# Optimization experiments

Hardware: AMD Instinct MI355X
Metric: run time of the kernel (lower is better)

## Reference

```python
import jax, jax.numpy as jnp
import numpy as np

B, T, E, U, V = 64, 100, 512, 512, 32000


def gru_layer(xs_tm, Wg, bg, Wc, bc):
    """TF GRUCell math. xs_tm: [T, B, D]. Returns (ys [T,B,U], h_final [B,U])."""
    u_dim = Wc.shape[1]
    h0 = jnp.zeros((xs_tm.shape[1], u_dim), xs_tm.dtype)

    def step(h, x):
        ru = jax.nn.sigmoid(jnp.concatenate([x, h], -1) @ Wg + bg)
        r, u = jnp.split(ru, 2, axis=-1)
        c = jnp.tanh(jnp.concatenate([x, r * h], -1) @ Wc + bc)
        h_new = u * h + (1.0 - u) * c
        return h_new, h_new

    h_final, ys = jax.lax.scan(step, h0, xs_tm)
    return ys, h_final


def setup_inputs() -> dict:
    key = jax.random.key(0)
    ks = jax.random.split(key, 16)

    def w(k, shape):
        fan_in = shape[0]
        return jax.random.normal(k, shape, jnp.float32) * (1.0 / np.sqrt(fan_in))

    inp = {
        "x": jax.random.randint(ks[0], (B, T), 0, V, jnp.int32),
        "embedding": jax.random.normal(ks[1], (V, E), jnp.float32) * 0.02,
        # bi-directional layer, input dim E
        "Wg_fw": w(ks[2], (E + U, 2 * U)), "bg_fw": jnp.ones((2 * U,), jnp.float32),
        "Wc_fw": w(ks[3], (E + U, U)),     "bc_fw": jnp.zeros((U,), jnp.float32),
        "Wg_bw": w(ks[4], (E + U, 2 * U)), "bg_bw": jnp.ones((2 * U,), jnp.float32),
        "Wc_bw": w(ks[5], (E + U, U)),     "bc_bw": jnp.zeros((U,), jnp.float32),
        # uni layer 1, input dim 2U (concat fw/bw)
        "Wg_u1": w(ks[6], (2 * U + U, 2 * U)), "bg_u1": jnp.ones((2 * U,), jnp.float32),
        "Wc_u1": w(ks[7], (2 * U + U, U)),     "bc_u1": jnp.zeros((U,), jnp.float32),
        # uni layer 2, input dim U
        "Wg_u2": w(ks[8], (U + U, 2 * U)), "bg_u2": jnp.ones((2 * U,), jnp.float32),
        "Wc_u2": w(ks[9], (U + U, U)),     "bc_u2": jnp.zeros((U,), jnp.float32),
    }
    return inp


def reference(x, embedding, Wg_fw, bg_fw, Wc_fw, bc_fw, Wg_bw, bg_bw, Wc_bw, bc_bw,
              Wg_u1, bg_u1, Wc_u1, bc_u1, Wg_u2, bg_u2, Wc_u2, bc_u2):
    emb = embedding[x]                      # [B, T, E] embedding lookup
    xs = jnp.swapaxes(emb, 0, 1)            # [T, B, E] time-major for scan
    # bidirectional GRU layer
    yf, _ = gru_layer(xs, Wg_fw, bg_fw, Wc_fw, bc_fw)
    yb, _ = gru_layer(xs[::-1], Wg_bw, bg_bw, Wc_bw, bc_bw)
    a = jnp.concatenate([yf, yb[::-1]], -1)  # [T, B, 2U]
    # 2-layer unidirectional GRU stack (MultiRNNCell)
    a, s1 = gru_layer(a, Wg_u1, bg_u1, Wc_u1, bc_u1)
    a, s2 = gru_layer(a, Wg_u2, bg_u2, Wc_u2, bc_u2)
    output = jnp.swapaxes(a, 0, 1)          # [B, T, U]
    state = jnp.stack([s1, s2])             # [2, B, U] per-layer final states
    return output, state
```

## Files before the change

### kernel.cpp

```cpp
#include <hip/hip_runtime.h>
#include <hip/hip_bf16.h>


#define TT 100

using f32x4 = __attribute__((ext_vector_type(4))) float;
using s16x8 = __attribute__((ext_vector_type(8))) short;
using u32x4 = __attribute__((ext_vector_type(4))) unsigned;

__device__ __forceinline__ unsigned short f2bfu(float x) {
  __hip_bfloat16 b = __float2bfloat16(x);
  unsigned short u;
  __builtin_memcpy(&u, &b, sizeof(u));
  return u;
}
__device__ __forceinline__ float bfu2f(unsigned short u) {
  __hip_bfloat16 b;
  __builtin_memcpy(&b, &u, sizeof(b));
  return __bfloat162float(b);
}
__device__ __forceinline__ float sigm(float x) {
  x = fminf(fmaxf(x, -30.f), 30.f);
  return 1.f / (1.f + __expf(-x));
}
__device__ __forceinline__ float tanh_fast(float x) {
  x = fminf(fmaxf(x, -15.f), 15.f);
  float e = __expf(-2.f * x);
  return (1.f - e) / (1.f + e);
}
__device__ __forceinline__ void vm_drain() {
  asm volatile("s_waitcnt vmcnt(0)" ::: "memory");
}

__global__ __launch_bounds__(256) void pack_w_kernel(const float* __restrict__ Wg,
                                                     const float* __restrict__ Wc,
                                                     int ldg, int ldc, int ktTot,
                                                     unsigned short* __restrict__ hi,
                                                     unsigned short* __restrict__ lo) {
  const int gg = blockIdx.x * 256 + threadIdx.x;
  if (gg >= 96 * ktTot * 64) return;
  const int lane = gg & 63;
  const int pair = gg >> 6;
  const int kt = pair % ktTot;
  const int nt = pair / ktTot;
  const int kg = lane >> 4;
  const int nl = lane & 15;
  const size_t off = (size_t)gg * 8;
  for (int i = 0; i < 8; ++i) {
    const int k = kt * 32 + kg * 8 + i;
    float v = (nt < 64) ? Wg[(size_t)k * ldg + nt * 16 + nl]
                        : Wc[(size_t)k * ldc + (nt - 64) * 16 + nl];
    unsigned short h = f2bfu(v);
    hi[off + i] = h;
    lo[off + i] = f2bfu(v - bfu2f(h));
  }
}

template <int ASRC>
__global__ __launch_bounds__(256) void gemm_mfma(
    const int* __restrict__ xtok, const float* __restrict__ emb,
    const unsigned short* __restrict__ aHi, const unsigned short* __restrict__ aLo, int lda,
    const unsigned short* __restrict__ bHi, const unsigned short* __restrict__ bLo,
    int ktTot, int ktX,
    const float* __restrict__ bg, const float* __restrict__ bc,
    float* __restrict__ C) {
  __shared__ unsigned short Ah[128 * 40];
  __shared__ unsigned short Al[128 * 40];

  const int tid = threadIdx.x;
  const int lane = tid & 63;
  const int w = tid >> 6;
  const int bm = blockIdx.x, bn = blockIdx.y;
  const int fm = lane & 15, fkg = lane >> 4;

  const int arow = tid >> 1;
  const int koff = (tid & 1) * 16;
  const int rowg = bm * 128 + arow;
  int embIdx = 0;
  if (ASRC == 0) {
    const int t_ = rowg >> 6, b_ = rowg & 63;
    embIdx = xtok[b_ * TT + t_];
  }

  f32x4 acc[2][8];
#pragma unroll
  for (int rt = 0; rt < 2; ++rt)
#pragma unroll
    for (int ni = 0; ni < 8; ++ni) acc[rt][ni] = (f32x4){0.f, 0.f, 0.f, 0.f};

  for (int kt = 0; kt < ktX; ++kt) {
    __syncthreads();
    if (ASRC == 0) {
      const float* src = emb + (size_t)embIdx * 512 + kt * 32 + koff;
      s16x8 h0, h1, l0, l1;
#pragma unroll
      for (int c = 0; c < 2; ++c) {
        f32x4 va = *(const f32x4*)(src + c * 8);
        f32x4 vb = *(const f32x4*)(src + c * 8 + 4);
        s16x8 hh, ll;
#pragma unroll
        for (int j = 0; j < 4; ++j) {
          unsigned short h = f2bfu(va[j]);
          hh[j] = (short)h; ll[j] = (short)f2bfu(va[j] - bfu2f(h));
          unsigned short h2 = f2bfu(vb[j]);
          hh[j + 4] = (short)h2; ll[j + 4] = (short)f2bfu(vb[j] - bfu2f(h2));
        }
        if (c == 0) { h0 = hh; l0 = ll; } else { h1 = hh; l1 = ll; }
      }
      *(s16x8*)(Ah + arow * 40 + koff) = h0;
      *(s16x8*)(Ah + arow * 40 + koff + 8) = h1;
      *(s16x8*)(Al + arow * 40 + koff) = l0;
      *(s16x8*)(Al + arow * 40 + koff + 8) = l1;
    } else {
      const size_t so = (size_t)rowg * lda + kt * 32 + koff;
      s16x8 h0 = *(const s16x8*)(aHi + so);
      s16x8 h1 = *(const s16x8*)(aHi + so + 8);
      s16x8 l0 = *(const s16x8*)(aLo + so);
      s16x8 l1 = *(const s16x8*)(aLo + so + 8);
      *(s16x8*)(Ah + arow * 40 + koff) = h0;
      *(s16x8*)(Ah + arow * 40 + koff + 8) = h1;
      *(s16x8*)(Al + arow * 40 + koff) = l0;
      *(s16x8*)(Al + arow * 40 + koff + 8) = l1;
    }
    __syncthreads();

    s16x8 ah[2], al[2];
#pragma unroll
    for (int rt = 0; rt < 2; ++rt) {
      const int m = w * 32 + rt * 16 + fm;
      ah[rt] = *(const s16x8*)(Ah + m * 40 + fkg * 8);
      al[rt] = *(const s16x8*)(Al + m * 40 + fkg * 8);
    }
#pragma unroll
    for (int ni = 0; ni < 8; ++ni) {
      const int nt = bn * 8 + ni;
      const size_t bo = ((size_t)nt * ktTot + kt) * 512 + lane * 8;
      s16x8 bh = *(const s16x8*)(bHi + bo);
      s16x8 bl = *(const s16x8*)(bLo + bo);
#pragma unroll
      for (int rt = 0; rt < 2; ++rt) {
        acc[rt][ni] = __builtin_amdgcn_mfma_f32_16x16x32_bf16(ah[rt], bh, acc[rt][ni], 0, 0, 0);
        acc[rt][ni] = __builtin_amdgcn_mfma_f32_16x16x32_bf16(ah[rt], bl, acc[rt][ni], 0, 0, 0);
        acc[rt][ni] = __builtin_amdgcn_mfma_f32_16x16x32_bf16(al[rt], bh, acc[rt][ni], 0, 0, 0);
      }
    }
  }

#pragma unroll
  for (int ni = 0; ni < 8; ++ni) {
    const int nt = bn * 8 + ni;
    int dcol; float bias;
    if (nt < 64) { dcol = nt * 16 + fm; bias = bg[dcol]; }
    else { dcol = 1024 + (nt - 64) * 16 + fm; bias = bc[(nt - 64) * 16 + fm]; }
#pragma unroll
    for (int rt = 0; rt < 2; ++rt)
#pragma unroll
      for (int j = 0; j < 4; ++j) {
        const int row = bm * 128 + w * 32 + rt * 16 + fkg * 4 + j;
        C[(size_t)row * 1536 + dcol] = acc[rt][ni][j] + bias;
      }
  }
}

template <int NB>
__global__ __launch_bounds__(256, 1) void gru_scan_kernel(
    const float* __restrict__ gxF, const float* __restrict__ gxB,
    const unsigned short* __restrict__ wHiF, const unsigned short* __restrict__ wLoF,
    const unsigned short* __restrict__ wHiB, const unsigned short* __restrict__ wLoB,
    int ktTot, int ktH0,
    unsigned* __restrict__ hPkG, unsigned* __restrict__ rPkG,
    unsigned* __restrict__ slots,
    unsigned short* __restrict__ yHi, unsigned short* __restrict__ yLo, int yld,
    float* __restrict__ outb,
    float* __restrict__ stout) {
  __shared__ unsigned short wHi_s[3 * 8192];
  __shared__ unsigned short wLo_s[3 * 8192];
  __shared__ float scr[4][16][17];
  __shared__ float scr2[4][16][17];

  const int tid = threadIdx.x;
  const int lane = tid & 63;
  const int wv = tid >> 6;
  const int bid = blockIdx.x;
  const int g = bid & 7;
  const int wg = bid >> 3;
  const int hs = wg << 4;

  int dir = 0, b0;
  const float* gx;
  const unsigned short *wph, *wpl;
  if (NB == 16) {
    dir = g & 1;
    b0 = (g >> 1) << 4;
    gx = dir ? gxB : gxF;
    wph = dir ? wHiB : wHiF;
    wpl = dir ? wLoB : wLoF;
  } else {
    b0 = g * NB;
    gx = gxF;
    wph = wHiF;
    wpl = wLoF;
  }

  {
    const int nt0[3] = {wg, 32 + wg, 64 + wg};
    for (int c = 0; c < 3; ++c) {
      const unsigned short* sH = wph + ((size_t)nt0[c] * ktTot + ktH0) * 512;
      const unsigned short* sL = wpl + ((size_t)nt0[c] * ktTot + ktH0) * 512;
      unsigned short* dH = wHi_s + c * 8192;
      unsigned short* dL = wLo_s + c * 8192;
#pragma unroll
      for (int it = 0; it < 4; ++it) {
        const int o = (it * 256 + tid) * 8;
        *(s16x8*)(dH + o) = *(const s16x8*)(sH + o);
        *(s16x8*)(dL + o) = *(const s16x8*)(sL + o);
      }
    }
  }
  __syncthreads();

  unsigned* gslots = slots + g * 32;

  const int fm = lane & 15;
  const int fkg = lane >> 4;
  const int afe = fm * 512;
  const int asw = (fm & 7) << 3;

  const int ob = tid >> 4, oj = tid & 15;
  const bool own = (ob < NB);
  const int ui = ob * 512 + ((hs + oj) ^ ((ob & 7) << 3));

  const size_t tileo = (size_t)g * 8192;

  auto mfma_regs = [&](int cidx, const s16x8* ah, const s16x8* al,
                       float (*dst)[16][17]) {
    f32x4 acc0 = {0.f, 0.f, 0.f, 0.f}, acc1 = {0.f, 0.f, 0.f, 0.f};
#pragma unroll
    for (int q = 0; q < 4; ++q) {
      const int kt = wv * 4 + q;
      const int wo = ((cidx * 16 + kt) * 64 + lane) * 8;
      s16x8 bh = *(const s16x8*)(wHi_s + wo);
      s16x8 bl = *(const s16x8*)(wLo_s + wo);
      if (q & 1) {
        acc1 = __builtin_amdgcn_mfma_f32_16x16x32_bf16(ah[q], bh, acc1, 0, 0, 0);
        acc1 = __builtin_amdgcn_mfma_f32_16x16x32_bf16(ah[q], bl, acc1, 0, 0, 0);
        acc1 = __builtin_amdgcn_mfma_f32_16x16x32_bf16(al[q], bh, acc1, 0, 0, 0);
      } else {
        acc0 = __builtin_amdgcn_mfma_f32_16x16x32_bf16(ah[q], bh, acc0, 0, 0, 0);
        acc0 = __builtin_amdgcn_mfma_f32_16x16x32_bf16(ah[q], bl, acc0, 0, 0, 0);
        acc0 = __builtin_amdgcn_mfma_f32_16x16x32_bf16(al[q], bh, acc0, 0, 0, 0);
      }
    }
#pragma unroll
    for (int j = 0; j < 4; ++j) dst[wv][fkg * 4 + j][fm] = acc0[j] + acc1[j];
  };

  auto load_frags = [&](const unsigned* pk, s16x8* ah, s16x8* al,
                        bool withHv, unsigned* hvOut) {
    u32x4 d[4][2];
#pragma unroll
    for (int q = 0; q < 4; ++q) {
      const int kt = wv * 4 + q;
      const unsigned* p = pk + tileo + afe + ((kt * 32 + fkg * 8) ^ asw);
      asm volatile("global_load_dwordx4 %0, %1, off sc0 sc1"
                   : "=v"(d[q][0]) : "v"(p) : "memory");
      asm volatile("global_load_dwordx4 %0, %1, off sc0 sc1"
                   : "=v"(d[q][1]) : "v"(p + 4) : "memory");
    }
    if (withHv && own)
      asm volatile("global_load_dword %0, %1, off sc0 sc1"
                   : "=v"(*hvOut) : "v"(pk + tileo + ui) : "memory");
    vm_drain();
    __builtin_amdgcn_sched_barrier(0);
#pragma unroll
    for (int q = 0; q < 4; ++q) {
      u32x4 hh, ll;
#pragma unroll
      for (int i = 0; i < 2; ++i) {
        const u32x4 dd = d[q][i];
        hh[2 * i] = (dd[0] & 0xffffu) | (dd[1] << 16);
        hh[2 * i + 1] = (dd[2] & 0xffffu) | (dd[3] << 16);
        ll[2 * i] = (dd[0] >> 16) | (dd[1] & 0xffff0000u);
        ll[2 * i + 1] = (dd[2] >> 16) | (dd[3] & 0xffff0000u);
      }
      __builtin_memcpy(&ah[q], &hh, 16);
      __builtin_memcpy(&al[q], &ll, 16);
    }
  };

  auto poll = [&](unsigned target) {
    if (tid < 32) {
      const unsigned* p = gslots + tid;
      unsigned v;
      do {
        asm volatile("global_load_dword %0, %1, off sc0 sc1\n\ts_waitcnt vmcnt(0)"
                     : "=v"(v) : "v"(p) : "memory");
      } while (!__all(v >= target));
    }
    __syncthreads();
  };

  float gxr = 0.f, gxu = 0.f, gxc = 0.f;
  if (own) {
    const float* row = gx + ((size_t)(dir ? TT - 1 : 0) * 64 + b0 + ob) * 1536 + hs + oj;
    gxr = row[0]; gxu = row[512]; gxc = row[1024];
  }

  for (int t = 0; t < TT; ++t) {
    const int tg = dir ? (TT - 1 - t) : t;

    s16x8 ah[4], al[4];
    unsigned hvu = 0;
    load_frags(hPkG, ah, al, true, &hvu);
    mfma_regs(0, ah, al, scr);
    __syncthreads();

    float hv = 0.f;
    if (own) {
      float rpre = scr[0][ob][oj] + scr[1][ob][oj] + scr[2][ob][oj] + scr[3][ob][oj] + gxr;
      float sg = sigm(rpre);
      hv = bfu2f((unsigned short)(hvu & 0xffffu)) + bfu2f((unsigned short)(hvu >> 16));
      float rh = sg * hv;
      unsigned short hh_ = f2bfu(rh);
      unsigned short ll_ = f2bfu(rh - bfu2f(hh_));
      unsigned e = (unsigned)hh_ | ((unsigned)ll_ << 16);
      asm volatile("global_store_dword %0, %1, off sc0 sc1"
                   :: "v"(rPkG + tileo + ui), "v"(e) : "memory");
    }
    vm_drain();
    __syncthreads();
    if (tid == 0) {
      unsigned tv = 2 * t + 1;
      asm volatile("global_store_dword %0, %1, off sc0 sc1"
                   :: "v"(gslots + wg), "v"(tv) : "memory");
    }

    mfma_regs(1, ah, al, scr2);

    float ngxr = 0.f, ngxu = 0.f, ngxc = 0.f;
    if (own && t + 1 < TT) {
      const int tgn = dir ? (TT - 2 - t) : (t + 1);
      const float* row = gx + ((size_t)tgn * 64 + b0 + ob) * 1536 + hs + oj;
      ngxr = row[0]; ngxu = row[512]; ngxc = row[1024];
    }

    poll(2 * t + 1);

    load_frags(rPkG, ah, al, false, nullptr);
    mfma_regs(2, ah, al, scr);
    __syncthreads();

    float hn = 0.f;
    unsigned short hh_ = 0, ll_ = 0;
    if (own) {
      float upre = scr2[0][ob][oj] + scr2[1][ob][oj] + scr2[2][ob][oj] + scr2[3][ob][oj] + gxu;
      float uv = sigm(upre);
      float cpre = scr[0][ob][oj] + scr[1][ob][oj] + scr[2][ob][oj] + scr[3][ob][oj] + gxc;
      float cv = tanh_fast(cpre);
      hn = uv * hv + (1.f - uv) * cv;
      hh_ = f2bfu(hn);
      ll_ = f2bfu(hn - bfu2f(hh_));
    }

    if (t == TT - 1) {
      if (own) {
        if (yHi) {
          const int ycol = (NB == 16) ? (dir * 512 + hs + oj) : (hs + oj);
          const size_t yi = ((size_t)tg * 64 + (b0 + ob)) * yld + ycol;
          yHi[yi] = hh_; yLo[yi] = ll_;
        }
        if (outb) outb[((size_t)(b0 + ob) * TT + t) * 512 + hs + oj] = hn;
        if (stout) stout[(size_t)(b0 + ob) * 512 + hs + oj] = hn;
      }
      break;
    }

    if (own) {
      unsigned e = (unsigned)hh_ | ((unsigned)ll_ << 16);
      asm volatile("global_store_dword %0, %1, off sc0 sc1"
                   :: "v"(hPkG + tileo + ui), "v"(e) : "memory");
    }
    vm_drain();
    __syncthreads();
    if (tid == 0) {
      unsigned tv = 2 * t + 2;
      asm volatile("global_store_dword %0, %1, off sc0 sc1"
                   :: "v"(gslots + wg), "v"(tv) : "memory");
    }

    if (own) {
      if (yHi) {
        const int ycol = (NB == 16) ? (dir * 512 + hs + oj) : (hs + oj);
        const size_t yi = ((size_t)tg * 64 + (b0 + ob)) * yld + ycol;
        yHi[yi] = hh_; yLo[yi] = ll_;
      }
      if (outb) outb[((size_t)(b0 + ob) * TT + t) * 512 + hs + oj] = hn;
    }
    gxr = ngxr; gxu = ngxu; gxc = ngxc;

    poll(2 * t + 2);
  }
}

extern "C" void kernel_launch(void* const* d_in, const int* in_sizes, int n_in,
                              void* d_out, int out_size, void* d_ws, size_t ws_size,
                              hipStream_t stream) {
  (void)in_sizes; (void)n_in; (void)out_size; (void)ws_size;
  const int* x = (const int*)d_in[0];
  const float* emb = (const float*)d_in[1];
  const float* WgFw = (const float*)d_in[2];
  const float* bgFw = (const float*)d_in[3];
  const float* WcFw = (const float*)d_in[4];
  const float* bcFw = (const float*)d_in[5];
  const float* WgBw = (const float*)d_in[6];
  const float* bgBw = (const float*)d_in[7];
  const float* WcBw = (const float*)d_in[8];
  const float* bcBw = (const float*)d_in[9];
  const float* WgU1 = (const float*)d_in[10];
  const float* bgU1 = (const float*)d_in[11];
  const float* WcU1 = (const float*)d_in[12];
  const float* bcU1 = (const float*)d_in[13];
  const float* WgU2 = (const float*)d_in[14];
  const float* bgU2 = (const float*)d_in[15];
  const float* WcU2 = (const float*)d_in[16];
  const float* bcU2 = (const float*)d_in[17];

  char* ws = (char*)d_ws;
  float* bufA = (float*)(ws + 0);
  float* bufB = (float*)(ws + 39321600);
  unsigned short* ycatHi = (unsigned short*)(ws + 78643200);
  unsigned short* ycatLo = (unsigned short*)(ws + 91750400);
  unsigned short* y1Hi = (unsigned short*)(ws + 78643200);
  unsigned short* y1Lo = (unsigned short*)(ws + 85196800);
  unsigned short* wpFwHi = (unsigned short*)(ws + 104857600);
  unsigned short* wpFwLo = (unsigned short*)(ws + 108003328);
  unsigned short* wpBwHi = (unsigned short*)(ws + 111149056);
  unsigned short* wpBwLo = (unsigned short*)(ws + 114294784);
  unsigned short* wpU1Hi = (unsigned short*)(ws + 117440512);
  unsigned short* wpU1Lo = (unsigned short*)(ws + 122159104);
  unsigned short* wpU2Hi = (unsigned short*)(ws + 117440512);
  unsigned short* wpU2Lo = (unsigned short*)(ws + 120586240);
  unsigned* hPkG = (unsigned*)(ws + 126877696);
  unsigned* rPkG = (unsigned*)(ws + 127139840);
  unsigned* bars = (unsigned*)(ws + 127401984);

  float* out = (float*)d_out;
  float* st1 = out + (size_t)64 * TT * 512;
  float* st2 = st1 + 64 * 512;

  hipMemsetAsync(bars, 0, 4096, stream);

  pack_w_kernel<<<768, 256, 0, stream>>>(WgFw, WcFw, 1024, 512, 32, wpFwHi, wpFwLo);
  pack_w_kernel<<<768, 256, 0, stream>>>(WgBw, WcBw, 1024, 512, 32, wpBwHi, wpBwLo);
  pack_w_kernel<<<1152, 256, 0, stream>>>(WgU1, WcU1, 1024, 512, 48, wpU1Hi, wpU1Lo);

  gemm_mfma<0><<<dim3(50, 12), 256, 0, stream>>>(
      x, emb, nullptr, nullptr, 0, wpFwHi, wpFwLo, 32, 16, bgFw, bcFw, bufA);
  gemm_mfma<0><<<dim3(50, 12), 256, 0, stream>>>(
      x, emb, nullptr, nullptr, 0, wpBwHi, wpBwLo, 32, 16, bgBw, bcBw, bufB);

  hipMemsetAsync(hPkG, 0, 524288, stream);
  {
    const float *a0 = bufA, *a1 = bufB;
    const unsigned short *w0 = wpFwHi, *w1 = wpFwLo, *w2 = wpBwHi, *w3 = wpBwLo;
    int ktT = 32, ktH = 16;
    unsigned *h0 = hPkG, *r0 = rPkG;
    unsigned* bp = bars;
    unsigned short *yh = ycatHi, *yl = ycatLo; int yld = 1024;
    float *on = nullptr, *sn = nullptr;
    void* args[] = {&a0, &a1, &w0, &w1, &w2, &w3, &ktT, &ktH, &h0, &r0,
                    &bp, &yh, &yl, &yld, &on, &sn};
    hipLaunchCooperativeKernel((const void*)gru_scan_kernel<16>, dim3(256), dim3(256),
                               args, 0, stream);
  }

  gemm_mfma<1><<<dim3(50, 12), 256, 0, stream>>>(
      nullptr, nullptr, ycatHi, ycatLo, 1024, wpU1Hi, wpU1Lo, 48, 32, bgU1, bcU1, bufA);

  hipMemsetAsync(hPkG, 0, 524288, stream);
  {
    const float *a0 = bufA, *a1 = nullptr;
    const unsigned short *w0 = wpU1Hi, *w1 = wpU1Lo, *w2 = nullptr, *w3 = nullptr;
    int ktT = 48, ktH = 32;
    unsigned *h0 = hPkG, *r0 = rPkG;
    unsigned* bp = bars + 256;
    unsigned short *yh = y1Hi, *yl = y1Lo; int yld = 512;
    float *on = nullptr, *sn = st1;
    void* args[] = {&a0, &a1, &w0, &w1, &w2, &w3, &ktT, &ktH, &h0, &r0,
                    &bp, &yh, &yl, &yld, &on, &sn};
    hipLaunchCooperativeKernel((const void*)gru_scan_kernel<8>, dim3(256), dim3(256),
                               args, 0, stream);
  }

  pack_w_kernel<<<768, 256, 0, stream>>>(WgU2, WcU2, 1024, 512, 32, wpU2Hi, wpU2Lo);

  gemm_mfma<1><<<dim3(50, 12), 256, 0, stream>>>(
      nullptr, nullptr, y1Hi, y1Lo, 512, wpU2Hi, wpU2Lo, 32, 16, bgU2, bcU2, bufB);

  hipMemsetAsync(hPkG, 0, 524288, stream);
  {
    const float *a0 = bufB, *a1 = nullptr;
    const unsigned short *w0 = wpU2Hi, *w1 = wpU2Lo, *w2 = nullptr, *w3 = nullptr;
    int ktT = 32, ktH = 16;
    unsigned *h0 = hPkG, *r0 = rPkG;
    unsigned* bp = bars + 512;
    unsigned short *yh = nullptr, *yl = nullptr; int yld = 0;
    float *on = out, *sn = st2;
    void* args[] = {&a0, &a1, &w0, &w1, &w2, &w3, &ktT, &ktH, &h0, &r0,
                    &bp, &yh, &yl, &yld, &on, &sn};
    hipLaunchCooperativeKernel((const void*)gru_scan_kernel<8>, dim3(256), dim3(256),
                               args, 0, stream);
  }
}
```

Before: 1.810 ms.

## Fuse the two unidirectional GRU layers into one wavefront-pipelined cooperative kernel

Replaces the separate layer-1 scan, layer-2 input GEMM and layer-2 scan with a single cooperative kernel. Half the blocks run layer 1 and the other half run layer 2, which polls layer-1 step flags and computes its input projection per timestep with global-memory weights. The layers thus overlap in a time-skewed pipeline, removing a full serial scan plus a GEMM launch. The cost is 128 blocks per layer instead of 256, extra per-step work for the fused input projection, and cross-layer flag polling latency.

```diff
diff --git a/kernel.cpp b/kernel.cpp
--- a/kernel.cpp
+++ b/kernel.cpp
@@ -30,6 +30,9 @@
 }
 __device__ __forceinline__ void vm_drain() {
   asm volatile("s_waitcnt vmcnt(0)" ::: "memory");
+}
+__device__ __forceinline__ void sc1_store_b16(void* p, unsigned v) {
+  asm volatile("global_store_short %0, %1, off sc0 sc1" :: "v"(p), "v"(v) : "memory");
 }
 
 __global__ __launch_bounds__(256) void pack_w_kernel(const float* __restrict__ Wg,
@@ -399,6 +402,324 @@
     gxr = ngxr; gxu = ngxu; gxc = ngxc;
 
     poll(2 * t + 2);
+  }
+}
+
+__global__ __launch_bounds__(256, 1) void uni_fused_kernel(
+    const float* __restrict__ gx1,
+    const unsigned short* __restrict__ w1Hi, const unsigned short* __restrict__ w1Lo,
+    const unsigned short* __restrict__ w2Hi, const unsigned short* __restrict__ w2Lo,
+    const float* __restrict__ bg2, const float* __restrict__ bc2,
+    unsigned* __restrict__ hPk1, unsigned* __restrict__ rPk1,
+    unsigned* __restrict__ hPk2, unsigned* __restrict__ rPk2,
+    unsigned* __restrict__ slots1, unsigned* __restrict__ slots2,
+    unsigned short* __restrict__ y1Hi, unsigned short* __restrict__ y1Lo,
+    float* __restrict__ out, float* __restrict__ st1, float* __restrict__ st2) {
+  __shared__ unsigned short wHi_s[3 * 8192];
+  __shared__ unsigned short wLo_s[3 * 8192];
+  __shared__ float scr[4][16][17];
+  __shared__ float scr2[4][16][17];
+  __shared__ float scr3[4][16][17];
+
+  const int tid = threadIdx.x;
+  const int lane = tid & 63;
+  const int wv = tid >> 6;
+  const int bid = blockIdx.x;
+  const int role = (bid >= 128);
+  const int g = (bid & 127) >> 5;
+  const int wg = bid & 31;
+  const int hs = wg << 4;
+  const int b0 = g * 16;
+
+  const unsigned short* wph = role ? w2Hi : w1Hi;
+  const unsigned short* wpl = role ? w2Lo : w1Lo;
+  const int ktTot = role ? 32 : 48;
+  const int ktH0 = role ? 16 : 32;
+  unsigned* hPk = role ? hPk2 : hPk1;
+  unsigned* rPk = role ? rPk2 : rPk1;
+  unsigned* myslots = (role ? slots2 : slots1) + g * 32;
+  unsigned* u1gs = slots1 + g * 32;
+
+  {
+    const int nt0[3] = {wg, 32 + wg, 64 + wg};
+    for (int c = 0; c < 3; ++c) {
+      const unsigned short* sH = wph + ((size_t)nt0[c] * ktTot + ktH0) * 512;
+      const unsigned short* sL = wpl + ((size_t)nt0[c] * ktTot + ktH0) * 512;
+      unsigned short* dH = wHi_s + c * 8192;
+      unsigned short* dL = wLo_s + c * 8192;
+#pragma unroll
+      for (int it = 0; it < 4; ++it) {
+        const int o = (it * 256 + tid) * 8;
+        *(s16x8*)(dH + o) = *(const s16x8*)(sH + o);
+        *(s16x8*)(dL + o) = *(const s16x8*)(sL + o);
+      }
+    }
+  }
+  __syncthreads();
+
+  const int fm = lane & 15;
+  const int fkg = lane >> 4;
+  const int afe = fm * 512;
+  const int asw = (fm & 7) << 3;
+  const int ob = tid >> 4, oj = tid & 15;
+  const int ui = ob * 512 + ((hs + oj) ^ ((ob & 7) << 3));
+  const size_t tileo = (size_t)g * 8192;
+
+  auto mfma_regs = [&](int cidx, const s16x8* ah, const s16x8* al,
+                       float (*dst)[16][17]) {
+    f32x4 acc0 = {0.f, 0.f, 0.f, 0.f}, acc1 = {0.f, 0.f, 0.f, 0.f};
+#pragma unroll
+    for (int q = 0; q < 4; ++q) {
+      const int kt = wv * 4 + q;
+      const int wo = ((cidx * 16 + kt) * 64 + lane) * 8;
+      s16x8 bh = *(const s16x8*)(wHi_s + wo);
+      s16x8 bl = *(const s16x8*)(wLo_s + wo);
+      if (q & 1) {
+        acc1 = __builtin_amdgcn_mfma_f32_16x16x32_bf16(ah[q], bh, acc1, 0, 0, 0);
+        acc1 = __builtin_amdgcn_mfma_f32_16x16x32_bf16(ah[q], bl, acc1, 0, 0, 0);
+        acc1 = __builtin_amdgcn_mfma_f32_16x16x32_bf16(al[q], bh, acc1, 0, 0, 0);
+      } else {
+        acc0 = __builtin_amdgcn_mfma_f32_16x16x32_bf16(ah[q], bh, acc0, 0, 0, 0);
+        acc0 = __builtin_amdgcn_mfma_f32_16x16x32_bf16(ah[q], bl, acc0, 0, 0, 0);
+        acc0 = __builtin_amdgcn_mfma_f32_16x16x32_bf16(al[q], bh, acc0, 0, 0, 0);
+      }
+    }
+#pragma unroll
+    for (int j = 0; j < 4; ++j) dst[wv][fkg * 4 + j][fm] = acc0[j] + acc1[j];
+  };
+
+  auto mfma_xp = [&](int cidx, const s16x8* ah, const s16x8* al,
+                     float (*dst)[16][17]) {
+    const int nt0[3] = {wg, 32 + wg, 64 + wg};
+    f32x4 acc0 = {0.f, 0.f, 0.f, 0.f}, acc1 = {0.f, 0.f, 0.f, 0.f};
+#pragma unroll
+    for (int q = 0; q < 4; ++q) {
+      const int kt = wv * 4 + q;
+      const size_t bo = ((size_t)nt0[cidx] * 32 + kt) * 512 + lane * 8;
+      s16x8 bh = *(const s16x8*)(w2Hi + bo);
+      s16x8 bl = *(const s16x8*)(w2Lo + bo);
+      if (q & 1) {
+        acc1 = __builtin_amdgcn_mfma_f32_16x16x32_bf16(ah[q], bh, acc1, 0, 0, 0);
+        acc1 = __builtin_amdgcn_mfma_f32_16x16x32_bf16(ah[q], bl, acc1, 0, 0, 0);
+        acc1 = __builtin_amdgcn_mfma_f32_16x16x32_bf16(al[q], bh, acc1, 0, 0, 0);
+      } else {
+        acc0 = __builtin_amdgcn_mfma_f32_16x16x32_bf16(ah[q], bh, acc0, 0, 0, 0);
+        acc0 = __builtin_amdgcn_mfma_f32_16x16x32_bf16(ah[q], bl, acc0, 0, 0, 0);
+        acc0 = __builtin_amdgcn_mfma_f32_16x16x32_bf16(al[q], bh, acc0, 0, 0, 0);
+      }
+    }
+#pragma unroll
+    for (int j = 0; j < 4; ++j) dst[wv][fkg * 4 + j][fm] = acc0[j] + acc1[j];
+  };
+
+  auto load_frags = [&](const unsigned* pk, s16x8* ah, s16x8* al,
+                        bool withHv, unsigned* hvOut) {
+    u32x4 d[4][2];
+#pragma unroll
+    for (int q = 0; q < 4; ++q) {
+      const int kt = wv * 4 + q;
+      const unsigned* p = pk + tileo + afe + ((kt * 32 + fkg * 8) ^ asw);
+      asm volatile("global_load_dwordx4 %0, %1, off sc0 sc1"
+                   : "=v"(d[q][0]) : "v"(p) : "memory");
+      asm volatile("global_load_dwordx4 %0, %1, off sc0 sc1"
+                   : "=v"(d[q][1]) : "v"(p + 4) : "memory");
+    }
+    if (withHv)
+      asm volatile("global_load_dword %0, %1, off sc0 sc1"
+                   : "=v"(*hvOut) : "v"(pk + tileo + ui) : "memory");
+    vm_drain();
+    __builtin_amdgcn_sched_barrier(0);
+#pragma unroll
+    for (int q = 0; q < 4; ++q) {
+      u32x4 hh, ll;
+#pragma unroll
+      for (int i = 0; i < 2; ++i) {
+        const u32x4 dd = d[q][i];
+        hh[2 * i] = (dd[0] & 0xffffu) | (dd[1] << 16);
+        hh[2 * i + 1] = (dd[2] & 0xffffu) | (dd[3] << 16);
+        ll[2 * i] = (dd[0] >> 16) | (dd[1] & 0xffff0000u);
+        ll[2 * i + 1] = (dd[2] >> 16) | (dd[3] & 0xffff0000u);
+      }
+      __builtin_memcpy(&ah[q], &hh, 16);
+      __builtin_memcpy(&al[q], &ll, 16);
+    }
+  };
+
+  auto poll_arr = [&](const unsigned* arr, unsigned target) {
+    if (tid < 32) {
+      const unsigned* p = arr + tid;
+      unsigned v;
+      do {
+        asm volatile("global_load_dword %0, %1, off sc0 sc1\n\ts_waitcnt vmcnt(0)"
+                     : "=v"(v) : "v"(p) : "memory");
+      } while (!__all(v >= target));
+    }
+    __syncthreads();
+  };
+
+  if (role == 0) {
+    float gxr, gxu, gxc;
+    {
+      const float* row = gx1 + ((size_t)0 * 64 + b0 + ob) * 1536 + hs + oj;
+      gxr = row[0]; gxu = row[512]; gxc = row[1024];
+    }
+    for (int t = 0; t < TT; ++t) {
+      s16x8 ah[4], al[4];
+      unsigned hvu = 0;
+      load_frags(hPk, ah, al, true, &hvu);
+      mfma_regs(0, ah, al, scr);
+      __syncthreads();
+
+      float rpre = scr[0][ob][oj] + scr[1][ob][oj] + scr[2][ob][oj] + scr[3][ob][oj] + gxr;
+      float sg = sigm(rpre);
+      float hv = bfu2f((unsigned short)(hvu & 0xffffu)) + bfu2f((unsigned short)(hvu >> 16));
+      float rh = sg * hv;
+      {
+        unsigned short hh_ = f2bfu(rh);
+        unsigned short ll_ = f2bfu(rh - bfu2f(hh_));
+        unsigned e = (unsigned)hh_ | ((unsigned)ll_ << 16);
+        asm volatile("global_store_dword %0, %1, off sc0 sc1"
+                     :: "v"(rPk + tileo + ui), "v"(e) : "memory");
+      }
+      vm_drain();
+      __syncthreads();
+      if (tid == 0) {
+        unsigned tv = 2 * t + 1;
+        asm volatile("global_store_dword %0, %1, off sc0 sc1"
+                     :: "v"(myslots + wg), "v"(tv) : "memory");
+      }
+
+      mfma_regs(1, ah, al, scr2);
+
+      float ngxr = 0.f, ngxu = 0.f, ngxc = 0.f;
+      if (t + 1 < TT) {
+        const float* row = gx1 + ((size_t)(t + 1) * 64 + b0 + ob) * 1536 + hs + oj;
+        ngxr = row[0]; ngxu = row[512]; ngxc = row[1024];
+      }
+
+      poll_arr(myslots, 2 * t + 1);
+
+      load_frags(rPk, ah, al, false, nullptr);
+      mfma_regs(2, ah, al, scr);
+      __syncthreads();
+
+      float upre = scr2[0][ob][oj] + scr2[1][ob][oj] + scr2[2][ob][oj] + scr2[3][ob][oj] + gxu;
+      float uv = sigm(upre);
+      float cpre = scr[0][ob][oj] + scr[1][ob][oj] + scr[2][ob][oj] + scr[3][ob][oj] + gxc;
+      float hn = uv * hv + (1.f - uv) * tanh_fast(cpre);
+      unsigned short hh_ = f2bfu(hn);
+      unsigned short ll_ = f2bfu(hn - bfu2f(hh_));
+
+      {
+        const size_t yi = ((size_t)t * 64 + (b0 + ob)) * 512 + hs + oj;
+        sc1_store_b16(y1Hi + yi, hh_);
+        sc1_store_b16(y1Lo + yi, ll_);
+      }
+      if (t < TT - 1) {
+        unsigned e = (unsigned)hh_ | ((unsigned)ll_ << 16);
+        asm volatile("global_store_dword %0, %1, off sc0 sc1"
+                     :: "v"(hPk + tileo + ui), "v"(e) : "memory");
+      } else {
+        st1[(size_t)(b0 + ob) * 512 + hs + oj] = hn;
+      }
+      vm_drain();
+      __syncthreads();
+      if (tid == 0) {
+        unsigned tv = 2 * t + 2;
+        asm volatile("global_store_dword %0, %1, off sc0 sc1"
+                     :: "v"(myslots + wg), "v"(tv) : "memory");
+      }
+      if (t == TT - 1) break;
+      gxr = ngxr; gxu = ngxu; gxc = ngxc;
+      poll_arr(myslots, 2 * t + 2);
+    }
+  } else {
+    const float br = bg2[hs + oj], bu = bg2[512 + hs + oj], bc_ = bc2[hs + oj];
+    for (int t = 0; t < TT; ++t) {
+      poll_arr(u1gs, 2 * t + 2);
+
+      s16x8 xh[4], xl[4];
+      {
+#pragma unroll
+        for (int q = 0; q < 4; ++q) {
+          const int kt = wv * 4 + q;
+          const size_t yo = ((size_t)t * 64 + b0 + fm) * 512 + kt * 32 + fkg * 8;
+          asm volatile("global_load_dwordx4 %0, %1, off sc0 sc1"
+                       : "=v"(xh[q]) : "v"(y1Hi + yo) : "memory");
+          asm volatile("global_load_dwordx4 %0, %1, off sc0 sc1"
+                       : "=v"(xl[q]) : "v"(y1Lo + yo) : "memory");
+        }
+        vm_drain();
+        __builtin_amdgcn_sched_barrier(0);
+      }
+      mfma_xp(0, xh, xl, scr);
+      mfma_xp(1, xh, xl, scr2);
+      mfma_xp(2, xh, xl, scr3);
+      __syncthreads();
+      float gxr = scr[0][ob][oj] + scr[1][ob][oj] + scr[2][ob][oj] + scr[3][ob][oj] + br;
+      float gxu = scr2[0][ob][oj] + scr2[1][ob][oj] + scr2[2][ob][oj] + scr2[3][ob][oj] + bu;
+      float gxc = scr3[0][ob][oj] + scr3[1][ob][oj] + scr3[2][ob][oj] + scr3[3][ob][oj] + bc_;
+      __syncthreads();
+
+      s16x8 ah[4], al[4];
+      unsigned hvu = 0;
+      load_frags(hPk, ah, al, true, &hvu);
+      mfma_regs(0, ah, al, scr);
+      __syncthreads();
+
+      float rpre = scr[0][ob][oj] + scr[1][ob][oj] + scr[2][ob][oj] + scr[3][ob][oj] + gxr;
+      float sg = sigm(rpre);
+      float hv = bfu2f((unsigned short)(hvu & 0xffffu)) + bfu2f((unsigned short)(hvu >> 16));
+      float rh = sg * hv;
+      {
+        unsigned short hh_ = f2bfu(rh);
+        unsigned short ll_ = f2bfu(rh - bfu2f(hh_));
+        unsigned e = (unsigned)hh_ | ((unsigned)ll_ << 16);
+        asm volatile("global_store_dword %0, %1, off sc0 sc1"
+                     :: "v"(rPk + tileo + ui), "v"(e) : "memory");
+      }
+      vm_drain();
+      __syncthreads();
+      if (tid == 0) {
+        unsigned tv = 2 * t + 1;
+        asm volatile("global_store_dword %0, %1, off sc0 sc1"
+                     :: "v"(myslots + wg), "v"(tv) : "memory");
+      }
+
+      mfma_regs(1, ah, al, scr2);
+      poll_arr(myslots, 2 * t + 1);
+
+      load_frags(rPk, ah, al, false, nullptr);
+      mfma_regs(2, ah, al, scr);
+      __syncthreads();
+
+      float upre = scr2[0][ob][oj] + scr2[1][ob][oj] + scr2[2][ob][oj] + scr2[3][ob][oj] + gxu;
+      float uv = sigm(upre);
+      float cpre = scr[0][ob][oj] + scr[1][ob][oj] + scr[2][ob][oj] + scr[3][ob][oj] + gxc;
+      float hn = uv * hv + (1.f - uv) * tanh_fast(cpre);
+
+      if (t == TT - 1) {
+        out[((size_t)(b0 + ob) * TT + t) * 512 + hs + oj] = hn;
+        st2[(size_t)(b0 + ob) * 512 + hs + oj] = hn;
+        break;
+      }
+      {
+        unsigned short hh_ = f2bfu(hn);
+        unsigned short ll_ = f2bfu(hn - bfu2f(hh_));
+        unsigned e = (unsigned)hh_ | ((unsigned)ll_ << 16);
+        asm volatile("global_store_dword %0, %1, off sc0 sc1"
+                     :: "v"(hPk + tileo + ui), "v"(e) : "memory");
+      }
+      vm_drain();
+      __syncthreads();
+      if (tid == 0) {
+        unsigned tv = 2 * t + 2;
+        asm volatile("global_store_dword %0, %1, off sc0 sc1"
+                     :: "v"(myslots + wg), "v"(tv) : "memory");
+      }
+      out[((size_t)(b0 + ob) * TT + t) * 512 + hs + oj] = hn;
+      poll_arr(myslots, 2 * t + 2);
+    }
   }
 }
 
@@ -438,11 +759,17 @@
   unsigned short* wpBwLo = (unsigned short*)(ws + 114294784);
   unsigned short* wpU1Hi = (unsigned short*)(ws + 117440512);
   unsigned short* wpU1Lo = (unsigned short*)(ws + 122159104);
-  unsigned short* wpU2Hi = (unsigned short*)(ws + 117440512);
-  unsigned short* wpU2Lo = (unsigned short*)(ws + 120586240);
-  unsigned* hPkG = (unsigned*)(ws + 126877696);
-  unsigned* rPkG = (unsigned*)(ws + 127139840);
+  unsigned short* wpU2Hi = (unsigned short*)(ws + 104857600);
+  unsigned short* wpU2Lo = (unsigned short*)(ws + 108003328);
+  unsigned* tiles = (unsigned*)(ws + 126877696);
   unsigned* bars = (unsigned*)(ws + 127401984);
+
+  unsigned* hPkB = tiles;
+  unsigned* rPkB = tiles + 65536;
+  unsigned* hPk1 = tiles;
+  unsigned* rPk1 = tiles + 32768;
+  unsigned* hPk2 = tiles + 65536;
+  unsigned* rPk2 = tiles + 98304;
 
   float* out = (float*)d_out;
   float* st1 = out + (size_t)64 * TT * 512;
@@ -459,12 +786,12 @@
   gemm_mfma<0><<<dim3(50, 12), 256, 0, stream>>>(
       x, emb, nullptr, nullptr, 0, wpBwHi, wpBwLo, 32, 16, bgBw, bcBw, bufB);
 
-  hipMemsetAsync(hPkG, 0, 524288, stream);
+  hipMemsetAsync(tiles, 0, 524288, stream);
   {
     const float *a0 = bufA, *a1 = bufB;
     const unsigned short *w0 = wpFwHi, *w1 = wpFwLo, *w2 = wpBwHi, *w3 = wpBwLo;
     int ktT = 32, ktH = 16;
-    unsigned *h0 = hPkG, *r0 = rPkG;
+    unsigned *h0 = hPkB, *r0 = rPkB;
     unsigned* bp = bars;
     unsigned short *yh = ycatHi, *yl = ycatLo; int yld = 1024;
     float *on = nullptr, *sn = nullptr;
@@ -474,41 +801,23 @@
                                args, 0, stream);
   }
 
+  pack_w_kernel<<<768, 256, 0, stream>>>(WgU2, WcU2, 1024, 512, 32, wpU2Hi, wpU2Lo);
+
   gemm_mfma<1><<<dim3(50, 12), 256, 0, stream>>>(
       nullptr, nullptr, ycatHi, ycatLo, 1024, wpU1Hi, wpU1Lo, 48, 32, bgU1, bcU1, bufA);
 
-  hipMemsetAsync(hPkG, 0, 524288, stream);
+  hipMemsetAsync(tiles, 0, 524288, stream);
   {
-    const float *a0 = bufA, *a1 = nullptr;
-    const unsigned short *w0 = wpU1Hi, *w1 = wpU1Lo, *w2 = nullptr, *w3 = nullptr;
-    int ktT = 48, ktH = 32;
-    unsigned *h0 = hPkG, *r0 = rPkG;
-    unsigned* bp = bars + 256;
-    unsigned short *yh = y1Hi, *yl = y1Lo; int yld = 512;
-    float *on = nullptr, *sn = st1;
-    void* args[] = {&a0, &a1, &w0, &w1, &w2, &w3, &ktT, &ktH, &h0, &r0,
-                    &bp, &yh, &yl, &yld, &on, &sn};
-    hipLaunchCooperativeKernel((const void*)gru_scan_kernel<8>, dim3(256), dim3(256),
+    const float* a0 = bufA;
+    const unsigned short *w0 = wpU1Hi, *w1 = wpU1Lo, *w2 = wpU2Hi, *w3 = wpU2Lo;
+    const float *b2 = bgU2, *c2 = bcU2;
+    unsigned *h1 = hPk1, *r1 = rPk1, *h2 = hPk2, *r2 = rPk2;
+    unsigned *s1p = bars + 256, *s2p = bars + 384;
+    unsigned short *yh = y1Hi, *yl = y1Lo;
+    float *op = out, *t1 = st1, *t2 = st2;
+    void* args[] = {&a0, &w0, &w1, &w2, &w3, &b2, &c2,
+                    &h1, &r1, &h2, &r2, &s1p, &s2p, &yh, &yl, &op, &t1, &t2};
+    hipLaunchCooperativeKernel((const void*)uni_fused_kernel, dim3(256), dim3(256),
                                args, 0, stream);
   }
-
-  pack_w_kernel<<<768, 256, 0, stream>>>(WgU2, WcU2, 1024, 512, 32, wpU2Hi, wpU2Lo);
-
-  gemm_mfma<1><<<dim3(50, 12), 256, 0, stream>>>(
-      nullptr, nullptr, y1Hi, y1Lo, 512, wpU2Hi, wpU2Lo, 32, 16, bgU2, bcU2, bufB);
-
-  hipMemsetAsync(hPkG, 0, 524288, stream);
-  {
-    const float *a0 = bufB, *a1 = nullptr;
-    const unsigned short *w0 = wpU2Hi, *w1 = wpU2Lo, *w2 = nullptr, *w3 = nullptr;
-    int ktT = 32, ktH = 16;
-    unsigned *h0 = hPkG, *r0 = rPkG;
-    unsigned* bp = bars + 512;
-    unsigned short *yh = nullptr, *yl = nullptr; int yld = 0;
-    float *on = out, *sn = st2;
-    void* args[] = {&a0, &a1, &w0, &w1, &w2, &w3, &ktT, &ktH, &h0, &r0,
-                    &bp, &yh, &yl, &yld, &on, &sn};
-    hipLaunchCooperativeKernel((const void*)gru_scan_kernel<8>, dim3(256), dim3(256),
-                               args, 0, stream);
-  }
-}
+}
```

Result: faster. 1.591 ms (-12.1%).
